# Kernel tuning notes

Hardware: AMD Instinct MI355X
Metric: run time of the kernel (lower is better)

The kernel has to match this reference:

```python
import jax, jax.numpy as jnp
import numpy as np

NUM_COMPONENTS = 32
RESOLUTION = 512
NUM_POINTS = 2_000_000


def setup_inputs() -> dict:
    key = jax.random.key(0)
    kp, k0, k1, k2 = jax.random.split(key, 4)
    # positions are grid_sample-style normalized coords in [-1, 1]
    positions = jax.random.uniform(kp, (NUM_POINTS, 3), jnp.float32, -1.0, 1.0)
    vec_x = jax.random.normal(k0, (NUM_COMPONENTS, RESOLUTION), jnp.float32)
    vec_y = jax.random.normal(k1, (NUM_COMPONENTS, RESOLUTION), jnp.float32)
    vec_z = jax.random.normal(k2, (NUM_COMPONENTS, RESOLUTION), jnp.float32)
    return {"positions": positions, "vec_x": vec_x, "vec_y": vec_y, "vec_z": vec_z}


def _sample_1d(vec, x):
    """1D bilinear lookup mimicking grid_sample(align_corners=True, padding='zeros').
    vec: [C, R] per-axis CP vectors; x: [N] coords in [-1, 1]. Returns [C, N]."""
    R = vec.shape[1]
    ix = (x + 1.0) * 0.5 * (R - 1)          # map [-1,1] -> [0, R-1]
    i0 = jnp.floor(ix)
    w1 = ix - i0                              # right-neighbor weight
    i0i = i0.astype(jnp.int32)
    i1i = i0i + 1

    def gather(idx):
        valid = (idx >= 0) & (idx < R)        # zero-padding outside the grid
        g = jnp.take(vec, jnp.clip(idx, 0, R - 1), axis=1)  # [C, N]
        return jnp.where(valid[None, :], g, 0.0)

    return gather(i0i) * (1.0 - w1)[None, :] + gather(i1i) * w1[None, :]


def reference(positions, vec_x, vec_y, vec_z):
    # positions: [..., 3]; unbind per axis, 1D-sample each CP vector set, product-reduce.
    batch_shape = positions.shape[:-1]
    flat = positions.reshape(-1, 3)
    fx = _sample_1d(vec_x, flat[:, 0])  # [C, N]
    fy = _sample_1d(vec_y, flat[:, 1])  # [C, N]
    fz = _sample_1d(vec_z, flat[:, 2])  # [C, N]
    feats = fx * fy * fz                 # elementwise product over axes, [C, N]
    return feats.T.reshape(*batch_shape, vec_x.shape[0])  # [..., C]
```

## Files before the change

### kernel.cpp

```cpp
#include <hip/hip_runtime.h>

#define NC 32
#define NR 512
#define HC 16
#define BLK 1024
#define PPB 1024
#define ITERS 4

#define LDS_FLOATS (3 * NR * HC)
#define LDS_BYTES (LDS_FLOATS * 4)

__global__ __launch_bounds__(256) void transpose_vecs(
    const float* __restrict__ vx, const float* __restrict__ vy,
    const float* __restrict__ vz, float* __restrict__ tx,
    float* __restrict__ ty, float* __restrict__ tz) {
  int u = blockIdx.x * 256 + threadIdx.x;
  if (u >= 3 * NC * NR) return;
  int table = u >> 14;
  int e = u & (NC * NR - 1);
  int c = e >> 9;
  int r = e & (NR - 1);
  const float* src = (table == 0) ? vx : (table == 1) ? vy : vz;
  float* dst = (table == 0) ? tx : (table == 1) ? ty : tz;
  dst[((c >> 4) << 13) + (r << 4) + (c & (HC - 1))] = src[e];
}

__device__ __forceinline__ float4 lerp4(const float* __restrict__ t,
                                        float x, int j4) {
  float ix = fmaf(x, 0.5f * (NR - 1), 0.5f * (NR - 1));
  ix = fminf(fmaxf(ix, 0.0f), (float)(NR - 1));
  float f = fminf(floorf(ix), (float)(NR - 2));
  float w = ix - f;
  int i0 = (int)f;
  const float* a = t + (i0 << 4) + j4;
  float4 v0 = *(const float4*)a;
  float4 v1 = *(const float4*)(a + HC);
  float4 r;
  r.x = fmaf(w, v1.x - v0.x, v0.x);
  r.y = fmaf(w, v1.y - v0.y, v0.y);
  r.z = fmaf(w, v1.z - v0.z, v0.z);
  r.w = fmaf(w, v1.w - v0.w, v0.w);
  return r;
}

__global__ __launch_bounds__(BLK, 4) void cp_encode_lds(
    const float* __restrict__ pos, const float* __restrict__ tx,
    const float* __restrict__ ty, const float* __restrict__ tz,
    float* __restrict__ out, int npts) {
  extern __shared__ float lds[];
  int tid = threadIdx.x;
  int base_p = blockIdx.x * PPB;
  int j4 = (tid & 3) << 2;
  int pofs = tid >> 2;

  float xs[ITERS], ys[ITERS], zs[ITERS];
  float4 r0[ITERS];
#pragma unroll
  for (int it = 0; it < ITERS; ++it) {
    int p = base_p + pofs + it * (BLK / 4);
    int pc = min(p, npts - 1);
    xs[it] = pos[3 * pc + 0];
    ys[it] = pos[3 * pc + 1];
    zs[it] = pos[3 * pc + 2];
  }

  for (int h = 0; h < 2; ++h) {
    __syncthreads();
    for (int u = tid; u < 3 * NR * 4; u += BLK) {
      int a = u >> 11;
      int rem = u & 2047;
      const float* src = (a == 0) ? tx : (a == 1) ? ty : tz;
      *(float4*)(&lds[(a << 13) + (rem << 2)]) =
          *(const float4*)(src + (h << 13) + (rem << 2));
    }
    __syncthreads();

#pragma unroll
    for (int it = 0; it < ITERS; ++it) {
      float4 fx = lerp4(lds, xs[it], j4);
      float4 fy = lerp4(lds + (NR * HC), ys[it], j4);
      float4 fz = lerp4(lds + 2 * (NR * HC), zs[it], j4);
      float4 r;
      r.x = fx.x * fy.x * fz.x;
      r.y = fx.y * fy.y * fz.y;
      r.z = fx.z * fy.z * fz.z;
      r.w = fx.w * fy.w * fz.w;
      if (h == 0) {
        r0[it] = r;
      } else {
        int p = base_p + pofs + it * (BLK / 4);
        if (p < npts) {
          float* o = out + (size_t)p * NC;
          *(float4*)(o + j4) = r0[it];
          *(float4*)(o + HC + j4) = r;
        }
      }
    }
  }
}

__device__ __forceinline__ float4 sample4_u(const float* __restrict__ t,
                                            float x, int c4) {
  float ix = (x + 1.0f) * 0.5f * (float)(NR - 1);
  float f = floorf(ix);
  float w = ix - f;
  int i0 = (int)f;
  int i1 = i0 + 1;
  float m0 = (i0 >= 0 && i0 < NR) ? (1.0f - w) : 0.0f;
  float m1 = (i1 >= 0 && i1 < NR) ? w : 0.0f;
  int ci0 = min(max(i0, 0), NR - 1);
  int ci1 = min(max(i1, 0), NR - 1);
  float4 r;
  float* rp = (float*)&r;
  for (int j = 0; j < 4; ++j) {
    float v0 = t[(c4 + j) * NR + ci0];
    float v1 = t[(c4 + j) * NR + ci1];
    rp[j] = v0 * m0 + v1 * m1;
  }
  return r;
}

__global__ __launch_bounds__(256) void cp_encode_global(
    const float* __restrict__ pos, const float* __restrict__ vx,
    const float* __restrict__ vy, const float* __restrict__ vz,
    float* __restrict__ out, int npts) {
  int t = blockIdx.x * 256 + threadIdx.x;
  int p = t >> 3;
  if (p >= npts) return;
  int c4 = (t & 7) * 4;
  float x = pos[3 * p + 0];
  float y = pos[3 * p + 1];
  float z = pos[3 * p + 2];
  float4 fx = sample4_u(vx, x, c4);
  float4 fy = sample4_u(vy, y, c4);
  float4 fz = sample4_u(vz, z, c4);
  float4 r;
  r.x = fx.x * fy.x * fz.x;
  r.y = fx.y * fy.y * fz.y;
  r.z = fx.z * fy.z * fz.z;
  r.w = fx.w * fy.w * fz.w;
  *(float4*)(out + (long long)p * NC + c4) = r;
}

extern "C" void kernel_launch(void* const* d_in, const int* in_sizes, int n_in,
                              void* d_out, int out_size, void* d_ws,
                              size_t ws_size, hipStream_t stream) {
  const float* pos = (const float*)d_in[0];
  const float* vx = (const float*)d_in[1];
  const float* vy = (const float*)d_in[2];
  const float* vz = (const float*)d_in[3];
  float* out = (float*)d_out;
  int npts = in_sizes[0] / 3;

  const size_t tbytes = (size_t)3 * NC * NR * sizeof(float);

  if (ws_size >= tbytes) {
    static int lds_attr_set = 0;
    if (!lds_attr_set) {
      hipFuncSetAttribute((const void*)cp_encode_lds,
                          hipFuncAttributeMaxDynamicSharedMemorySize,
                          LDS_BYTES);
      lds_attr_set = 1;
    }
    float* tx = (float*)d_ws;
    float* ty = tx + NC * NR;
    float* tz = ty + NC * NR;
    int tb = (3 * NC * NR + 255) / 256;
    transpose_vecs<<<tb, 256, 0, stream>>>(vx, vy, vz, tx, ty, tz);
    int blocks = (npts + PPB - 1) / PPB;
    cp_encode_lds<<<blocks, BLK, LDS_BYTES, stream>>>(pos, tx, ty, tz, out,
                                                      npts);
  } else {
    int blocks = (npts * 8 + 255) / 256;
    cp_encode_global<<<blocks, 256, 0, stream>>>(pos, vx, vy, vz, out, npts);
  }
}
```

Baseline: 318.2 us.

## Fuse table transpose into main kernel with padded LDS rows

Drops the separate transpose kernel. Each block now reads the original [C,R] vectors directly and scatters them into LDS in row-major form, with the row stride padded to 20 floats to reduce bank conflicts. Index and weight computation is hoisted out of the two-half loop so it runs once per point. The trade-off is that every block redoes the transpose through scalar LDS stores, and the LDS footprint per block grows by 25%, which may reduce occupancy.

```diff
diff --git a/kernel.cpp b/kernel.cpp
--- a/kernel.cpp
+++ b/kernel.cpp
@@ -7,34 +7,24 @@
 #define PPB 1024
 #define ITERS 4
 
-#define LDS_FLOATS (3 * NR * HC)
+#define RS 20
+#define AXW (NR * RS)
+#define LDS_FLOATS (3 * AXW)
 #define LDS_BYTES (LDS_FLOATS * 4)
 
-__global__ __launch_bounds__(256) void transpose_vecs(
-    const float* __restrict__ vx, const float* __restrict__ vy,
-    const float* __restrict__ vz, float* __restrict__ tx,
-    float* __restrict__ ty, float* __restrict__ tz) {
-  int u = blockIdx.x * 256 + threadIdx.x;
-  if (u >= 3 * NC * NR) return;
-  int table = u >> 14;
-  int e = u & (NC * NR - 1);
-  int c = e >> 9;
-  int r = e & (NR - 1);
-  const float* src = (table == 0) ? vx : (table == 1) ? vy : vz;
-  float* dst = (table == 0) ? tx : (table == 1) ? ty : tz;
-  dst[((c >> 4) << 13) + (r << 4) + (c & (HC - 1))] = src[e];
+__device__ __forceinline__ void idxw(float x, int j4, int axbase,
+                                     int* off, float* w) {
+  float ix = fmaf(x, 255.5f, 255.5f);
+  ix = fminf(fmaxf(ix, 0.0f), 511.0f);
+  float f = fminf(floorf(ix), 510.0f);
+  *w = ix - f;
+  *off = axbase + (int)f * RS + j4;
 }
 
-__device__ __forceinline__ float4 lerp4(const float* __restrict__ t,
-                                        float x, int j4) {
-  float ix = fmaf(x, 0.5f * (NR - 1), 0.5f * (NR - 1));
-  ix = fminf(fmaxf(ix, 0.0f), (float)(NR - 1));
-  float f = fminf(floorf(ix), (float)(NR - 2));
-  float w = ix - f;
-  int i0 = (int)f;
-  const float* a = t + (i0 << 4) + j4;
-  float4 v0 = *(const float4*)a;
-  float4 v1 = *(const float4*)(a + HC);
+__device__ __forceinline__ float4 lerp4w(const float* __restrict__ lds,
+                                         int off, float w) {
+  float4 v0 = *(const float4*)(lds + off);
+  float4 v1 = *(const float4*)(lds + off + RS);
   float4 r;
   r.x = fmaf(w, v1.x - v0.x, v0.x);
   r.y = fmaf(w, v1.y - v0.y, v0.y);
@@ -43,43 +33,54 @@
   return r;
 }
 
-__global__ __launch_bounds__(BLK, 4) void cp_encode_lds(
-    const float* __restrict__ pos, const float* __restrict__ tx,
-    const float* __restrict__ ty, const float* __restrict__ tz,
+__global__ __launch_bounds__(BLK, 4) void cp_encode_fused(
+    const float* __restrict__ pos, const float* __restrict__ vx,
+    const float* __restrict__ vy, const float* __restrict__ vz,
     float* __restrict__ out, int npts) {
   extern __shared__ float lds[];
-  int tid = threadIdx.x;
-  int base_p = blockIdx.x * PPB;
-  int j4 = (tid & 3) << 2;
-  int pofs = tid >> 2;
+  const int tid = threadIdx.x;
+  const int base_p = blockIdx.x * PPB;
+  const int j4 = (tid & 3) << 2;
+  const int pofs = tid >> 2;
 
-  float xs[ITERS], ys[ITERS], zs[ITERS];
-  float4 r0[ITERS];
+  int offx[ITERS], offy[ITERS], offz[ITERS];
+  float wx[ITERS], wy[ITERS], wz[ITERS];
 #pragma unroll
   for (int it = 0; it < ITERS; ++it) {
     int p = base_p + pofs + it * (BLK / 4);
     int pc = min(p, npts - 1);
-    xs[it] = pos[3 * pc + 0];
-    ys[it] = pos[3 * pc + 1];
-    zs[it] = pos[3 * pc + 2];
+    float x = pos[3 * pc + 0];
+    float y = pos[3 * pc + 1];
+    float z = pos[3 * pc + 2];
+    idxw(x, j4, 0, &offx[it], &wx[it]);
+    idxw(y, j4, AXW, &offy[it], &wy[it]);
+    idxw(z, j4, 2 * AXW, &offz[it], &wz[it]);
   }
 
+  float4 r0[ITERS];
+
+#pragma unroll
   for (int h = 0; h < 2; ++h) {
     __syncthreads();
-    for (int u = tid; u < 3 * NR * 4; u += BLK) {
+    for (int u = tid; u < 3 * 2048; u += BLK) {
       int a = u >> 11;
-      int rem = u & 2047;
-      const float* src = (a == 0) ? tx : (a == 1) ? ty : tz;
-      *(float4*)(&lds[(a << 13) + (rem << 2)]) =
-          *(const float4*)(src + (h << 13) + (rem << 2));
+      int c = u & 15;
+      int m = (u >> 4) & 127;
+      const float* src = (a == 0) ? vx : (a == 1) ? vy : vz;
+      float4 v = *(const float4*)(src + (h << 13) + (c << 9) + (m << 2));
+      int wbase = a * AXW + (m << 2) * RS + c;
+      lds[wbase + 0 * RS] = v.x;
+      lds[wbase + 1 * RS] = v.y;
+      lds[wbase + 2 * RS] = v.z;
+      lds[wbase + 3 * RS] = v.w;
     }
     __syncthreads();
 
 #pragma unroll
     for (int it = 0; it < ITERS; ++it) {
-      float4 fx = lerp4(lds, xs[it], j4);
-      float4 fy = lerp4(lds + (NR * HC), ys[it], j4);
-      float4 fz = lerp4(lds + 2 * (NR * HC), zs[it], j4);
+      float4 fx = lerp4w(lds, offx[it], wx[it]);
+      float4 fy = lerp4w(lds, offy[it], wy[it]);
+      float4 fz = lerp4w(lds, offz[it], wz[it]);
       float4 r;
       r.x = fx.x * fy.x * fz.x;
       r.y = fx.y * fy.y * fz.y;
@@ -99,49 +100,6 @@
   }
 }
 
-__device__ __forceinline__ float4 sample4_u(const float* __restrict__ t,
-                                            float x, int c4) {
-  float ix = (x + 1.0f) * 0.5f * (float)(NR - 1);
-  float f = floorf(ix);
-  float w = ix - f;
-  int i0 = (int)f;
-  int i1 = i0 + 1;
-  float m0 = (i0 >= 0 && i0 < NR) ? (1.0f - w) : 0.0f;
-  float m1 = (i1 >= 0 && i1 < NR) ? w : 0.0f;
-  int ci0 = min(max(i0, 0), NR - 1);
-  int ci1 = min(max(i1, 0), NR - 1);
-  float4 r;
-  float* rp = (float*)&r;
-  for (int j = 0; j < 4; ++j) {
-    float v0 = t[(c4 + j) * NR + ci0];
-    float v1 = t[(c4 + j) * NR + ci1];
-    rp[j] = v0 * m0 + v1 * m1;
-  }
-  return r;
-}
-
-__global__ __launch_bounds__(256) void cp_encode_global(
-    const float* __restrict__ pos, const float* __restrict__ vx,
-    const float* __restrict__ vy, const float* __restrict__ vz,
-    float* __restrict__ out, int npts) {
-  int t = blockIdx.x * 256 + threadIdx.x;
-  int p = t >> 3;
-  if (p >= npts) return;
-  int c4 = (t & 7) * 4;
-  float x = pos[3 * p + 0];
-  float y = pos[3 * p + 1];
-  float z = pos[3 * p + 2];
-  float4 fx = sample4_u(vx, x, c4);
-  float4 fy = sample4_u(vy, y, c4);
-  float4 fz = sample4_u(vz, z, c4);
-  float4 r;
-  r.x = fx.x * fy.x * fz.x;
-  r.y = fx.y * fy.y * fz.y;
-  r.z = fx.z * fy.z * fz.z;
-  r.w = fx.w * fy.w * fz.w;
-  *(float4*)(out + (long long)p * NC + c4) = r;
-}
-
 extern "C" void kernel_launch(void* const* d_in, const int* in_sizes, int n_in,
                               void* d_out, int out_size, void* d_ws,
                               size_t ws_size, hipStream_t stream) {
@@ -151,27 +109,17 @@
   const float* vz = (const float*)d_in[3];
   float* out = (float*)d_out;
   int npts = in_sizes[0] / 3;
+  if (npts <= 0) return;
 
-  const size_t tbytes = (size_t)3 * NC * NR * sizeof(float);
-
-  if (ws_size >= tbytes) {
-    static int lds_attr_set = 0;
-    if (!lds_attr_set) {
-      hipFuncSetAttribute((const void*)cp_encode_lds,
-                          hipFuncAttributeMaxDynamicSharedMemorySize,
-                          LDS_BYTES);
-      lds_attr_set = 1;
-    }
-    float* tx = (float*)d_ws;
-    float* ty = tx + NC * NR;
-    float* tz = ty + NC * NR;
-    int tb = (3 * NC * NR + 255) / 256;
-    transpose_vecs<<<tb, 256, 0, stream>>>(vx, vy, vz, tx, ty, tz);
-    int blocks = (npts + PPB - 1) / PPB;
-    cp_encode_lds<<<blocks, BLK, LDS_BYTES, stream>>>(pos, tx, ty, tz, out,
+  static int lds_attr_set = 0;
+  if (!lds_attr_set) {
+    hipFuncSetAttribute((const void*)cp_encode_fused,
+                        hipFuncAttributeMaxDynamicSharedMemorySize, LDS_BYTES);
+    lds_attr_set = 1;
+  }
+  int blocks = (npts + PPB - 1) / PPB;
+  cp_encode_fused<<<blocks, BLK, LDS_BYTES, stream>>>(pos, vx, vy, vz, out,
                                                       npts);
-  } else {
-    int blocks = (npts * 8 + 255) / 256;
-    cp_encode_global<<<blocks, 256, 0, stream>>>(pos, vx, vy, vz, out, npts);
-  }
+  (void)d_ws;
+  (void)ws_size;
 }
```

Result: slower. 337.2 us (+6.0%).

## Stage one padded axis table at a time via direct global-to-LDS loads

Applied to the files above, without the earlier changes.

The tables are re-laid out as row-major [R][36] padded images, so each row holds all 32 channels with padding meant to reduce bank conflicts. The kernel now stages one axis table (72KB) at a time into LDS using global_load_lds and multiplies the per-axis lerps into an accumulator. Each thread handles 4 channels for 8 threads per point, and the full 128-byte row is written at the end. Blocks shrink to 512 threads with 512 points each. Every block still loads 216KB of tables per 512 points, which doubles table traffic per point compared with before. There are also three sync-separated phases.

```diff
diff --git a/kernel.cpp b/kernel.cpp
--- a/kernel.cpp
+++ b/kernel.cpp
@@ -2,18 +2,17 @@
 
 #define NC 32
 #define NR 512
-#define HC 16
-#define BLK 1024
-#define PPB 1024
-#define ITERS 4
+#define BLK 512
+#define PPB 512
+#define PTS_PER_IT (BLK / 8)
+#define ITERS (PPB / PTS_PER_IT)
+#define RS 36
+#define AXW (NR * RS)
+#define LDS_BYTES (AXW * 4)
 
-#define LDS_FLOATS (3 * NR * HC)
-#define LDS_BYTES (LDS_FLOATS * 4)
-
-__global__ __launch_bounds__(256) void transpose_vecs(
+__global__ __launch_bounds__(256) void make_images(
     const float* __restrict__ vx, const float* __restrict__ vy,
-    const float* __restrict__ vz, float* __restrict__ tx,
-    float* __restrict__ ty, float* __restrict__ tz) {
+    const float* __restrict__ vz, float* __restrict__ ws) {
   int u = blockIdx.x * 256 + threadIdx.x;
   if (u >= 3 * NC * NR) return;
   int table = u >> 14;
@@ -21,81 +20,75 @@
   int c = e >> 9;
   int r = e & (NR - 1);
   const float* src = (table == 0) ? vx : (table == 1) ? vy : vz;
-  float* dst = (table == 0) ? tx : (table == 1) ? ty : tz;
-  dst[((c >> 4) << 13) + (r << 4) + (c & (HC - 1))] = src[e];
+  ws[table * AXW + r * RS + c] = src[e];
 }
 
-__device__ __forceinline__ float4 lerp4(const float* __restrict__ t,
-                                        float x, int j4) {
-  float ix = fmaf(x, 0.5f * (NR - 1), 0.5f * (NR - 1));
-  ix = fminf(fmaxf(ix, 0.0f), (float)(NR - 1));
-  float f = fminf(floorf(ix), (float)(NR - 2));
-  float w = ix - f;
-  int i0 = (int)f;
-  const float* a = t + (i0 << 4) + j4;
-  float4 v0 = *(const float4*)a;
-  float4 v1 = *(const float4*)(a + HC);
-  float4 r;
-  r.x = fmaf(w, v1.x - v0.x, v0.x);
-  r.y = fmaf(w, v1.y - v0.y, v0.y);
-  r.z = fmaf(w, v1.z - v0.z, v0.z);
-  r.w = fmaf(w, v1.w - v0.w, v0.w);
-  return r;
-}
-
-__global__ __launch_bounds__(BLK, 4) void cp_encode_lds(
-    const float* __restrict__ pos, const float* __restrict__ tx,
-    const float* __restrict__ ty, const float* __restrict__ tz,
+__global__ __launch_bounds__(BLK, 4) void cp_encode(
+    const float* __restrict__ pos, const float* __restrict__ ws,
     float* __restrict__ out, int npts) {
   extern __shared__ float lds[];
-  int tid = threadIdx.x;
-  int base_p = blockIdx.x * PPB;
-  int j4 = (tid & 3) << 2;
-  int pofs = tid >> 2;
+  const int tid = threadIdx.x;
+  const int base_p = blockIdx.x * PPB;
+  const int j4 = (tid & 7) << 2;
+  const int pofs = tid >> 3;
 
-  float xs[ITERS], ys[ITERS], zs[ITERS];
-  float4 r0[ITERS];
+  float px[ITERS], py[ITERS], pz[ITERS];
 #pragma unroll
   for (int it = 0; it < ITERS; ++it) {
-    int p = base_p + pofs + it * (BLK / 4);
+    int p = base_p + pofs + it * PTS_PER_IT;
     int pc = min(p, npts - 1);
-    xs[it] = pos[3 * pc + 0];
-    ys[it] = pos[3 * pc + 1];
-    zs[it] = pos[3 * pc + 2];
+    px[it] = pos[3 * pc + 0];
+    py[it] = pos[3 * pc + 1];
+    pz[it] = pos[3 * pc + 2];
   }
 
-  for (int h = 0; h < 2; ++h) {
+  float4 acc[ITERS];
+
+#pragma unroll
+  for (int a = 0; a < 3; ++a) {
     __syncthreads();
-    for (int u = tid; u < 3 * NR * 4; u += BLK) {
-      int a = u >> 11;
-      int rem = u & 2047;
-      const float* src = (a == 0) ? tx : (a == 1) ? ty : tz;
-      *(float4*)(&lds[(a << 13) + (rem << 2)]) =
-          *(const float4*)(src + (h << 13) + (rem << 2));
+    const float* g = ws + a * AXW;
+#pragma unroll
+    for (int k = 0; k < 9; ++k) {
+      int o = (k * BLK + tid) << 2;
+      __builtin_amdgcn_global_load_lds(
+          (const __attribute__((address_space(1))) unsigned int*)(g + o),
+          (__attribute__((address_space(3))) unsigned int*)(lds + o),
+          16, 0, 0);
     }
     __syncthreads();
 
 #pragma unroll
     for (int it = 0; it < ITERS; ++it) {
-      float4 fx = lerp4(lds, xs[it], j4);
-      float4 fy = lerp4(lds + (NR * HC), ys[it], j4);
-      float4 fz = lerp4(lds + 2 * (NR * HC), zs[it], j4);
-      float4 r;
-      r.x = fx.x * fy.x * fz.x;
-      r.y = fx.y * fy.y * fz.y;
-      r.z = fx.z * fy.z * fz.z;
-      r.w = fx.w * fy.w * fz.w;
-      if (h == 0) {
-        r0[it] = r;
+      float x = (a == 0) ? px[it] : (a == 1) ? py[it] : pz[it];
+      float ix = fmaf(x, 255.5f, 255.5f);
+      ix = fminf(fmaxf(ix, 0.0f), 511.0f);
+      float f = fminf(floorf(ix), 510.0f);
+      float w = ix - f;
+      const float* adr = lds + (int)f * RS + j4;
+      float4 v0 = *(const float4*)adr;
+      float4 v1 = *(const float4*)(adr + RS);
+      float4 s;
+      s.x = fmaf(w, v1.x - v0.x, v0.x);
+      s.y = fmaf(w, v1.y - v0.y, v0.y);
+      s.z = fmaf(w, v1.z - v0.z, v0.z);
+      s.w = fmaf(w, v1.w - v0.w, v0.w);
+      if (a == 0) {
+        acc[it] = s;
       } else {
-        int p = base_p + pofs + it * (BLK / 4);
-        if (p < npts) {
-          float* o = out + (size_t)p * NC;
-          *(float4*)(o + j4) = r0[it];
-          *(float4*)(o + HC + j4) = r;
-        }
+        acc[it].x *= s.x;
+        acc[it].y *= s.y;
+        acc[it].z *= s.z;
+        acc[it].w *= s.w;
       }
     }
+  }
+
+#pragma unroll
+  for (int it = 0; it < ITERS; ++it) {
+    int p = base_p + pofs + it * PTS_PER_IT;
+    if (p < npts)
+      *(float4*)(out + (size_t)p * NC + j4) = acc[it];
   }
 }
 
@@ -151,25 +144,23 @@
   const float* vz = (const float*)d_in[3];
   float* out = (float*)d_out;
   int npts = in_sizes[0] / 3;
+  if (npts <= 0) return;
 
-  const size_t tbytes = (size_t)3 * NC * NR * sizeof(float);
+  const size_t ibytes = (size_t)3 * AXW * sizeof(float);
 
-  if (ws_size >= tbytes) {
+  if (ws_size >= ibytes) {
     static int lds_attr_set = 0;
     if (!lds_attr_set) {
-      hipFuncSetAttribute((const void*)cp_encode_lds,
+      hipFuncSetAttribute((const void*)cp_encode,
                           hipFuncAttributeMaxDynamicSharedMemorySize,
                           LDS_BYTES);
       lds_attr_set = 1;
     }
-    float* tx = (float*)d_ws;
-    float* ty = tx + NC * NR;
-    float* tz = ty + NC * NR;
+    float* ws = (float*)d_ws;
     int tb = (3 * NC * NR + 255) / 256;
-    transpose_vecs<<<tb, 256, 0, stream>>>(vx, vy, vz, tx, ty, tz);
+    make_images<<<tb, 256, 0, stream>>>(vx, vy, vz, ws);
     int blocks = (npts + PPB - 1) / PPB;
-    cp_encode_lds<<<blocks, BLK, LDS_BYTES, stream>>>(pos, tx, ty, tz, out,
-                                                      npts);
+    cp_encode<<<blocks, BLK, LDS_BYTES, stream>>>(pos, ws, out, npts);
   } else {
     int blocks = (npts * 8 + 255) / 256;
     cp_encode_global<<<blocks, 256, 0, stream>>>(pos, vx, vy, vz, out, npts);
```

New measurement: 576.0 us. 1.81x slower.
